# Kernel tuning notes

Measured on AMD Instinct MI355X. Metric: run time of the kernel, lower is better.

The kernel has to match this reference:

```python
import jax, jax.numpy as jnp
from jax import lax
import numpy as np


def _conv2d(x, w, b, pad):
    # x: NCHW, w: OIHW
    o = lax.conv_general_dilated(x, w, window_strides=(1, 1),
                                 padding=[(pad, pad), (pad, pad)],
                                 dimension_numbers=('NCHW', 'OIHW', 'NCHW'))
    return o + b[None, :, None, None]


def _maxpool(x, kh, kw):
    return lax.reduce_window(x, -jnp.inf, lax.max,
                             window_dimensions=(1, 1, kh, kw),
                             window_strides=(1, 1, kh, kw),
                             padding='VALID')


def _l2norm(x, axis):
    n = jnp.sqrt(jnp.sum(x * x, axis=axis, keepdims=True))
    return x / jnp.maximum(n, 1e-12)


def setup_inputs() -> dict:
    key = jax.random.key(0)
    ks = jax.random.split(key, 12)
    d = {}
    d['x'] = jax.random.normal(ks[0], (16, 128, 40, 200), dtype=jnp.float32)
    d['cluster_centers'] = jax.random.uniform(ks[1], (64, 128), dtype=jnp.float32)
    d['conv_w'] = jax.random.normal(ks[2], (64, 128, 1, 1), dtype=jnp.float32) * 0.05
    d['conv_b'] = jax.random.normal(ks[3], (64,), dtype=jnp.float32) * 0.05
    d['w1'] = jax.random.normal(ks[4], (256, 128, 5, 5), dtype=jnp.float32) * 0.02
    d['b1'] = jax.random.normal(ks[5], (256,), dtype=jnp.float32) * 0.02
    d['w2'] = jax.random.normal(ks[6], (512, 256, 5, 5), dtype=jnp.float32) * 0.02
    d['b2'] = jax.random.normal(ks[7], (512,), dtype=jnp.float32) * 0.02
    d['w3'] = jax.random.normal(ks[8], (1024, 512, 5, 5), dtype=jnp.float32) * 0.02
    d['b3'] = jax.random.normal(ks[9], (1024,), dtype=jnp.float32) * 0.02
    d['mlp_w'] = jax.random.normal(ks[10], (256, 9216), dtype=jnp.float32) * 0.01
    d['mlp_b'] = jax.random.normal(ks[11], (256,), dtype=jnp.float32) * 0.01
    return d


def reference(x, cluster_centers, conv_w, conv_b, w1, b1, w2, b2, w3, b3, mlp_w, mlp_b):
    N, C, H, W = x.shape
    K = conv_w.shape[0]
    P = H * W

    # soft assignment: 1x1 conv -> softmax over cluster axis
    sa = _conv2d(x, conv_w, conv_b, 0).reshape(N, K, P)
    a = jax.nn.softmax(sa, axis=1)                      # [N, K, P]

    x_flat = x.reshape(N, C, P)
    # sum_p a[n,k,p] * (x[n,c,p] - centers[k,c])  -- algebraically equal to
    # the explicit NxKxCxP residual tensor, computed without materializing it.
    vlad = jnp.einsum('nkp,ncp->nkc', a, x_flat) \
           - a.sum(axis=-1)[:, :, None] * cluster_centers[None, :, :]
    vlad = _l2norm(vlad, axis=2)                        # intra-norm per cluster
    vlad = _l2norm(vlad.reshape(N, K * C), axis=1)      # [N, K*C]

    # CNN branch
    h = _conv2d(x, w1, b1, 2)
    h = jnp.where(h >= 0, h, 0.2 * h)                   # LeakyReLU(0.2)
    h = _maxpool(h, 2, 2)
    h = _conv2d(h, w2, b2, 2)
    h = jnp.where(h >= 0, h, 0.2 * h)
    h = _maxpool(h, 4, 4)
    h = _conv2d(h, w3, b3, 2)
    h = _maxpool(h, 5, 25)                              # -> [N, 1024, 1, 1]
    x_feat = _l2norm(h.reshape(N, -1), axis=1)          # [N, 1024]

    feat = jnp.concatenate([vlad, x_feat], axis=1)      # [N, 9216]
    out = feat @ mlp_w.T + mlp_b
    return _l2norm(out, axis=1)
```

## Files before the change

### kernel.cpp

```cpp
#include <hip/hip_runtime.h>
#include <math.h>

#define K_ 64
#define C_ 128
#define NB 16
#define P_ 8000

typedef float f32x4 __attribute__((ext_vector_type(4)));
typedef short s16x8 __attribute__((ext_vector_type(8)));

__device__ __forceinline__ short f2bf(float v) {
    unsigned u = __float_as_uint(v);
    u += 0x7FFFu + ((u >> 16) & 1u);
    return (short)(u >> 16);
}
__device__ __forceinline__ float bf2f(ushort u) { return __uint_as_float(((unsigned)u) << 16); }

__device__ __forceinline__ void stage16(const void* g, void* l) {
    __builtin_amdgcn_global_load_lds(
        (const __attribute__((address_space(1))) void*)g,
        (__attribute__((address_space(3))) void*)l, 16, 0, 0);
}

__global__ void k_transpose_tiled(const float* __restrict__ in, float* __restrict__ out,
                                  int Co, int E)
{
    __shared__ float t[32][33];
    const int e0  = blockIdx.x * 32;
    const int co0 = blockIdx.y * 32;
    for (int i = threadIdx.y; i < 32; i += 8) {
        int co = co0 + i, e = e0 + threadIdx.x;
        t[i][threadIdx.x] = (co < Co && e < E) ? in[(size_t)co * E + e] : 0.f;
    }
    __syncthreads();
    for (int i = threadIdx.y; i < 32; i += 8) {
        int e = e0 + i, co = co0 + threadIdx.x;
        if (e < E && co < Co) out[(size_t)e * Co + co] = t[threadIdx.x][i];
    }
}

__global__ void k_nchw_to_nhwc(const float* __restrict__ in, ushort* __restrict__ out,
                               int C, int P)
{
    __shared__ ushort t[32][33];
    const int n  = blockIdx.z;
    const int p0 = blockIdx.x * 32;
    const int c0 = blockIdx.y * 32;
    for (int i = threadIdx.y; i < 32; i += 8) {
        int c = c0 + i, p = p0 + threadIdx.x;
        t[i][threadIdx.x] = (c < C && p < P) ? (ushort)f2bf(in[((size_t)n * C + c) * P + p]) : 0;
    }
    __syncthreads();
    for (int i = threadIdx.y; i < 32; i += 8) {
        int p = p0 + i, c = c0 + threadIdx.x;
        if (p < P && c < C) out[((size_t)n * P + p) * C + c] = t[threadIdx.x][i];
    }
}

__global__ void k_wprep(const float* __restrict__ w, short* __restrict__ wb,
                        int Co, int Cin, int total)
{
    int idx = blockIdx.x * blockDim.x + threadIdx.x;
    if (idx >= total) return;
    int cl = idx & 31;
    int rest = idx >> 5;
    int co = rest % Co;
    int rest2 = rest / Co;
    int t = rest2 % 25;
    int ck = rest2 / 25;
    float v = w[((size_t)co * Cin + (ck << 5) + cl) * 25 + t];
    wb[idx] = f2bf(v);
}

template<int SR, int NC, int WR, int WC16, int IS3>
__global__ __launch_bounds__(256) void k_conv_mfma(
    const ushort* __restrict__ in, const s16x8* __restrict__ wb,
    const float* __restrict__ bias, ushort* __restrict__ outb, float* __restrict__ outf,
    const ushort* __restrict__ zg,
    int Cin, int Co, int H, int W, int WT, int leaky, int nck, int xpc, int PT)
{
    constexpr int NT   = IS3 ? 4 : (WR * WC16);
    constexpr int TOT  = SR * NC * 4;
    constexpr int TOTP = (TOT + 63) & ~63;
    __shared__ s16x8 xin[TOTP];
    __shared__ s16x8 wl[2][4][256];

    const int tid  = threadIdx.x;
    const int lane = tid & 63;
    const int wid  = tid >> 6;
    const int wm   = wid >> 1;
    const int wn   = wid & 1;
    const int n16  = lane & 15;
    const int g    = lane >> 4;

    const int lid  = blockIdx.x;
    const int xcd  = lid & 7;
    const int rrr  = lid >> 3;
    const int co_blk = xcd / xpc;
    const int posn = rrr * xpc + (xcd % xpc);
    const int n    = posn / PT;
    const int bx   = posn % PT;

    const int h0  = IS3 ? 0 : (bx / WT) * (2 * WR);
    const int w0  = IS3 ? 0 : (bx % WT) * (WC16 * 16);
    const int ks  = IS3 ? bx : 0;
    const int co0 = co_blk * 128;

    int ph[NT], pw[NT];
    if (IS3) {
        #pragma unroll
        for (int nt = 0; nt < NT; ++nt) {
            int pos = wn * 64 + nt * 16 + n16;
            int h = pos / 25;
            int w = pos - h * 25;
            if (h > 4) { h = 0; w = 0; }
            ph[nt] = h; pw[nt] = w;
        }
    }

    f32x4 acc[4][NT];
    #pragma unroll
    for (int i = 0; i < 4; ++i)
        #pragma unroll
        for (int j = 0; j < NT; ++j) acc[i][j] = f32x4{0.f, 0.f, 0.f, 0.f};

    const int ck0 = IS3 ? ks * nck : 0;
    const int ckend = ck0 + nck;

    auto stage_input = [&](int ck) {
        for (int c = wid; c * 64 < TOTP; c += 4) {
            int u = c * 64 + lane;
            int row = u / (NC * 4);
            int rem = u - row * (NC * 4);
            int col = rem >> 2;
            int s   = rem & 3;
            int g8  = (s - (col >> 1) - row) & 3;
            int gh = h0 + row - 2, gw = w0 + col - 2;
            const void* src =
                (u < TOT && (unsigned)gh < (unsigned)H && (unsigned)gw < (unsigned)W)
                ? (const void*)(in + ((size_t)(n * H + gh) * W + gw) * Cin + (ck << 5) + (g8 << 3))
                : (const void*)zg;
            stage16(src, (void*)&xin[c * 64]);
        }
    };
    auto stage_w = [&](int gT, int slot) {
        const s16x8* src = wb + ((size_t)gT * Co + co0 + wm * 64) * 4 + lane;
        #pragma unroll
        for (int k = 0; k < 4; ++k)
            stage16((const void*)(src + k * 64), (void*)&wl[slot][wid][k * 64]);
    };

    for (int ck = ck0; ck < ckend; ++ck) {
        if (ck != ck0) __builtin_amdgcn_s_barrier();
        stage_input(ck);
        stage_w(ck * 25, 0);
        asm volatile("s_waitcnt vmcnt(4)" ::: "memory");
        __builtin_amdgcn_sched_barrier(0);
        __builtin_amdgcn_s_barrier();

        #pragma unroll
        for (int t = 0; t < 25; ++t) {
            if (t < 24) {
                stage_w(ck * 25 + t + 1, (t + 1) & 1);
                asm volatile("s_waitcnt vmcnt(4)" ::: "memory");
            } else {
                asm volatile("s_waitcnt vmcnt(0)" ::: "memory");
            }
            __builtin_amdgcn_sched_barrier(0);

            const int r = t / 5, s = t - (t / 5) * 5;

            const s16x8* wt_ = &wl[t & 1][wid][n16 * 4 + g];
            s16x8 wf[4];
            #pragma unroll
            for (int mt = 0; mt < 4; ++mt) wf[mt] = wt_[mt * 64];

            s16x8 bf[NT];
            #pragma unroll
            for (int nt = 0; nt < NT; ++nt) {
                int row, col;
                if (IS3) { row = ph[nt] + r; col = pw[nt] + s; }
                else {
                    int rr = nt / WC16, cc = nt - rr * WC16;
                    row = wn * WR + rr + r;
                    col = cc * 16 + n16 + s;
                }
                bf[nt] = xin[(row * NC + col) * 4 + ((g + (col >> 1) + row) & 3)];
            }
            #pragma unroll
            for (int mt = 0; mt < 4; ++mt)
                #pragma unroll
                for (int nt = 0; nt < NT; ++nt)
                    acc[mt][nt] = __builtin_amdgcn_mfma_f32_16x16x32_bf16(
                        wf[mt], bf[nt], acc[mt][nt], 0, 0, 0);
        }
    }

    if (IS3) {
        #pragma unroll
        for (int mt = 0; mt < 4; ++mt) {
            #pragma unroll
            for (int reg = 0; reg < 4; ++reg) {
                const int co = co0 + wm * 64 + mt * 16 + g * 4 + reg;
                #pragma unroll
                for (int nt = 0; nt < NT; ++nt) {
                    int pos = wn * 64 + nt * 16 + n16;
                    if (pos < 125)
                        outf[((size_t)(ks * NB + n) * Co + co) * 125 + pos] = acc[mt][nt][reg];
                }
            }
        }
    } else {
        #pragma unroll
        for (int mt = 0; mt < 4; ++mt) {
            const int cobase = co0 + wm * 64 + mt * 16 + g * 4;
            const float b0 = bias[cobase + 0];
            const float b1 = bias[cobase + 1];
            const float b2 = bias[cobase + 2];
            const float b3 = bias[cobase + 3];
            #pragma unroll
            for (int nt = 0; nt < NT; ++nt) {
                int rr = nt / WC16, cc = nt - rr * WC16;
                int h  = h0 + wn * WR + rr;
                int wp = w0 + cc * 16 + n16;
                if (h < H && wp < W) {
                    float v0 = acc[mt][nt][0] + b0;
                    float v1 = acc[mt][nt][1] + b1;
                    float v2 = acc[mt][nt][2] + b2;
                    float v3 = acc[mt][nt][3] + b3;
                    if (leaky) {
                        v0 = (v0 >= 0.f) ? v0 : 0.2f * v0;
                        v1 = (v1 >= 0.f) ? v1 : 0.2f * v1;
                        v2 = (v2 >= 0.f) ? v2 : 0.2f * v2;
                        v3 = (v3 >= 0.f) ? v3 : 0.2f * v3;
                    }
                    ushort4 pkd;
                    pkd.x = (ushort)f2bf(v0);
                    pkd.y = (ushort)f2bf(v1);
                    pkd.z = (ushort)f2bf(v2);
                    pkd.w = (ushort)f2bf(v3);
                    *(ushort4*)(outb + ((size_t)(n * H + h) * W + wp) * Co + cobase) = pkd;
                }
            }
        }
    }
}

__global__ __launch_bounds__(256) void k_vlad_partial(
    const float* __restrict__ x,
    const float* __restrict__ convw_t,
    const float* __restrict__ convb,
    float* __restrict__ pv,
    float* __restrict__ pa)
{
    __shared__ float xs[C_][64];
    __shared__ float als[64][K_];
    __shared__ float pgsum[4][K_];

    const int tid = threadIdx.x;
    const int chunk = blockIdx.x;
    const int n = blockIdx.y;
    const int p0 = chunk * 64;

    const float* xn = x + (size_t)n * C_ * P_ + p0;
    for (int i = tid; i < C_ * 64; i += 256) {
        int c = i >> 6, pp = i & 63;
        xs[c][pp] = xn[(size_t)c * P_ + pp];
    }
    __syncthreads();

    const int k  = tid & 63;
    const int pg = tid >> 6;

    float sa[16];
    const float bk = convb[k];
    #pragma unroll
    for (int j = 0; j < 16; ++j) sa[j] = bk;
    for (int c = 0; c < C_; ++c) {
        float wv = convw_t[c * K_ + k];
        const float4* xp = (const float4*)&xs[c][pg * 16];
        #pragma unroll
        for (int q = 0; q < 4; ++q) {
            float4 xv = xp[q];
            sa[q*4+0] += wv * xv.x;
            sa[q*4+1] += wv * xv.y;
            sa[q*4+2] += wv * xv.z;
            sa[q*4+3] += wv * xv.w;
        }
    }

    float asum_loc = 0.f;
    #pragma unroll
    for (int j = 0; j < 16; ++j) {
        float m = sa[j];
        for (int d = 32; d >= 1; d >>= 1) m = fmaxf(m, __shfl_xor(m, d));
        float e = __expf(sa[j] - m);
        float s = e;
        for (int d = 32; d >= 1; d >>= 1) s += __shfl_xor(s, d);
        float a = e / s;
        als[pg * 16 + j][k] = a;
        asum_loc += a;
    }
    pgsum[pg][k] = asum_loc;
    __syncthreads();
    if (tid < K_) {
        pa[((size_t)n * 125 + chunk) * K_ + tid] =
            pgsum[0][tid] + pgsum[1][tid] + pgsum[2][tid] + pgsum[3][tid];
    }

    const int q = pg;
    float acc[32];
    #pragma unroll
    for (int j = 0; j < 32; ++j) acc[j] = 0.f;
    for (int p = 0; p < 64; p += 4) {
        float a0 = als[p+0][k], a1 = als[p+1][k], a2 = als[p+2][k], a3 = als[p+3][k];
        #pragma unroll
        for (int j = 0; j < 32; ++j) {
            const float4 xv = *(const float4*)&xs[q*32 + j][p];
            acc[j] += a0*xv.x + a1*xv.y + a2*xv.z + a3*xv.w;
        }
    }
    float* pvp = pv + ((((size_t)n * 125 + chunk) * K_ + k) * C_ + q * 32);
    #pragma unroll
    for (int j = 0; j < 32; ++j) pvp[j] = acc[j];
}

__global__ void k_vlad_reduce(const float* __restrict__ pv, float* __restrict__ vlad_raw)
{
    int idx = blockIdx.x * blockDim.x + threadIdx.x;
    if (idx >= NB * 8192) return;
    int n = idx >> 13;
    int rest = idx & 8191;
    const float* p = pv + (size_t)n * 125 * 8192 + rest;
    float s = 0.f;
    for (int ch = 0; ch < 125; ++ch) s += p[(size_t)ch * 8192];
    vlad_raw[(size_t)n * 8192 + rest] = s;
}

__global__ void k_asum_reduce(const float* __restrict__ pa, float* __restrict__ asum)
{
    int idx = blockIdx.x * blockDim.x + threadIdx.x;
    if (idx >= NB * K_) return;
    const float* p = pa + (size_t)(idx >> 6) * 125 * K_ + (idx & 63);
    float s = 0.f;
    for (int ch = 0; ch < 125; ++ch) s += p[ch * K_];
    asum[idx] = s;
}

__global__ __launch_bounds__(128) void k_vlad_finalize(
    const float* __restrict__ vlad_raw, const float* __restrict__ asum,
    const float* __restrict__ centers, float* __restrict__ feat)
{
    __shared__ float red[2];
    const int k = blockIdx.x, n = blockIdx.y, c = threadIdx.x;
    float v = vlad_raw[((size_t)n * K_ + k) * C_ + c] - asum[n * K_ + k] * centers[k * C_ + c];
    float ss = v * v;
    for (int d = 32; d >= 1; d >>= 1) ss += __shfl_xor(ss, d);
    if ((threadIdx.x & 63) == 0) red[threadIdx.x >> 6] = ss;
    __syncthreads();
    float denom = fmaxf(sqrtf(red[0] + red[1]), 1e-12f);
    feat[(size_t)n * 9216 + k * C_ + c] = v / denom;
}

__global__ void k_maxpool_cl(const ushort* __restrict__ in, ushort* __restrict__ out,
                             int Hi, int Wi, int C8, int ph, int pw, int total)
{
    int idx = blockIdx.x * blockDim.x + threadIdx.x;
    if (idx >= total) return;
    const int Ho = Hi / ph, Wo = Wi / pw;
    const int C = C8 << 3;
    int c8 = idx % C8;
    int t  = idx / C8;
    int wo = t % Wo; t /= Wo;
    int ho = t % Ho;
    int n  = t / Ho;
    const ushort* base = in + ((size_t)(n * Hi + ho * ph) * Wi + wo * pw) * C + (c8 << 3);
    float m[8];
    #pragma unroll
    for (int j = 0; j < 8; ++j) m[j] = -INFINITY;
    for (int r = 0; r < ph; ++r)
        for (int s = 0; s < pw; ++s) {
            s16x8 v = *(const s16x8*)(base + ((size_t)r * Wi + s) * C);
            #pragma unroll
            for (int j = 0; j < 8; ++j) m[j] = fmaxf(m[j], bf2f((ushort)v[j]));
        }
    s16x8 o;
    #pragma unroll
    for (int j = 0; j < 8; ++j) o[j] = f2bf(m[j]);
    *(s16x8*)(out + ((size_t)(n * Ho + ho) * Wo + wo) * C + (c8 << 3)) = o;
}

__global__ void k_pool3_feat(const float* __restrict__ part, const float* __restrict__ bias,
                             float* __restrict__ feat)
{
    int idx = blockIdx.x * blockDim.x + threadIdx.x;
    if (idx >= NB * 1024) return;
    int n = idx >> 10, c = idx & 1023;
    const size_t kstride = (size_t)NB * 1024 * 125;
    const float* p0 = part + ((size_t)n * 1024 + c) * 125;
    const float* p1 = p0 + kstride;
    const float* p2 = p1 + kstride;
    const float* p3 = p2 + kstride;
    const float b = bias[c];
    float m = -INFINITY;
    for (int i = 0; i < 125; ++i)
        m = fmaxf(m, b + ((p0[i] + p1[i]) + (p2[i] + p3[i])));
    feat[(size_t)n * 9216 + 8192 + c] = m;
}

__global__ __launch_bounds__(256) void k_featnorm(const float* __restrict__ feat,
                                                  float* __restrict__ scale)
{
    __shared__ float r1s[4], r2s[4];
    const int n = blockIdx.x;
    const int tid = threadIdx.x;
    const int wid = tid >> 6;
    float s1 = 0.f, s2 = 0.f;
    const float* f = feat + (size_t)n * 9216;
    for (int i = tid; i < 9216; i += 256) {
        float v = f[i];
        if (i < 8192) s1 += v * v; else s2 += v * v;
    }
    for (int d = 32; d >= 1; d >>= 1) { s1 += __shfl_xor(s1, d); s2 += __shfl_xor(s2, d); }
    if ((tid & 63) == 0) { r1s[wid] = s1; r2s[wid] = s2; }
    __syncthreads();
    if (tid == 0) {
        scale[n * 2 + 0] = 1.f / fmaxf(sqrtf(r1s[0] + r1s[1] + r1s[2] + r1s[3]), 1e-12f);
        scale[n * 2 + 1] = 1.f / fmaxf(sqrtf(r2s[0] + r2s[1] + r2s[2] + r2s[3]), 1e-12f);
    }
}

__global__ __launch_bounds__(256) void k_mlp_part(
    const float* __restrict__ feat, const float* __restrict__ scale,
    const float* __restrict__ wt,
    float* __restrict__ part)
{
    __shared__ float fs[576];
    const int n  = blockIdx.x >> 4;
    const int sl = blockIdx.x & 15;
    const int tid = threadIdx.x;
    const int base = sl * 576;
    for (int j = tid; j < 576; j += 256) {
        int idx = base + j;
        fs[j] = feat[(size_t)n * 9216 + idx] * scale[n * 2 + (idx < 8192 ? 0 : 1)];
    }
    __syncthreads();
    float a0 = 0.f, a1 = 0.f;
    for (int j = 0; j < 576; j += 2) {
        a0 += fs[j]     * wt[(size_t)(base + j)     * 256 + tid];
        a1 += fs[j + 1] * wt[(size_t)(base + j + 1) * 256 + tid];
    }
    part[((size_t)n * 16 + sl) * 256 + tid] = a0 + a1;
}

__global__ __launch_bounds__(256) void k_mlp_final(
    const float* __restrict__ part, const float* __restrict__ bias,
    float* __restrict__ outp)
{
    __shared__ float red[4];
    const int n = blockIdx.x;
    const int tid = threadIdx.x;
    float a = bias[tid];
    #pragma unroll
    for (int s = 0; s < 16; ++s) a += part[((size_t)n * 16 + s) * 256 + tid];
    float ss = a * a;
    for (int d = 32; d >= 1; d >>= 1) ss += __shfl_xor(ss, d);
    if ((tid & 63) == 0) red[tid >> 6] = ss;
    __syncthreads();
    const float inv = 1.f / fmaxf(sqrtf(red[0] + red[1] + red[2] + red[3]), 1e-12f);
    outp[n * 256 + tid] = a * inv;
}

extern "C" void kernel_launch(void* const* d_in, const int* in_sizes, int n_in,
                              void* d_out, int out_size, void* d_ws, size_t ws_size,
                              hipStream_t stream)
{
    const float* x      = (const float*)d_in[0];
    const float* cents  = (const float*)d_in[1];
    const float* conv_w = (const float*)d_in[2];
    const float* conv_b = (const float*)d_in[3];
    const float* w1     = (const float*)d_in[4];
    const float* b1     = (const float*)d_in[5];
    const float* w2     = (const float*)d_in[6];
    const float* b2     = (const float*)d_in[7];
    const float* w3     = (const float*)d_in[8];
    const float* b3     = (const float*)d_in[9];
    const float* mlp_w  = (const float*)d_in[10];
    const float* mlp_b  = (const float*)d_in[11];
    float* outp = (float*)d_out;

    char* ws = (char*)d_ws;
    size_t off = 0;
    auto alloc = [&](size_t bytes) -> void* {
        off = (off + 255) & ~(size_t)255;
        void* p = ws + off;
        off += bytes;
        return p;
    };
    ushort* zguard  = (ushort*)alloc(256);
    float*  convw_t = (float*)alloc((size_t)64 * 128 * 4);
    float*  mwt     = (float*)alloc((size_t)9216 * 256 * 4);
    short*  wb1     = (short*)alloc((size_t)819200 * 2);
    short*  wb2     = (short*)alloc((size_t)3276800 * 2);
    short*  wb3     = (short*)alloc((size_t)13107200 * 2);
    ushort* x_cl    = (ushort*)alloc((size_t)NB * 8000 * 128 * 2);
    float*  vlad_raw= (float*)alloc((size_t)NB * 8192 * 4);
    float*  asum    = (float*)alloc((size_t)NB * K_ * 4);
    float*  feat    = (float*)alloc((size_t)NB * 9216 * 4);
    float*  pa      = (float*)alloc((size_t)NB * 125 * K_ * 4);
    float*  scale   = (float*)alloc((size_t)NB * 2 * 4);
    float*  mpart   = (float*)alloc((size_t)NB * 16 * 256 * 4);
    ushort* pool2b  = (ushort*)alloc((size_t)NB * 125 * 512 * 2);
    float*  part3   = (float*)alloc((size_t)4 * NB * 1024 * 125 * 4);
    char*   slabA   = (char*)alloc((size_t)NB * 8000 * 256 * 2);
    ushort* slabB   = (ushort*)alloc((size_t)NB * 2000 * 256 * 2);

    hipMemsetAsync(zguard, 0, 256, stream);

    {
        dim3 blk(32, 8);
        k_transpose_tiled<<<dim3(4, 2), blk, 0, stream>>>(conv_w, convw_t, 64, 128);
        k_transpose_tiled<<<dim3(288, 8), blk, 0, stream>>>(mlp_w, mwt, 256, 9216);
        k_wprep<<<(819200 + 255) / 256, 256, 0, stream>>>(w1, wb1, 256, 128, 819200);
        k_wprep<<<(3276800 + 255) / 256, 256, 0, stream>>>(w2, wb2, 512, 256, 3276800);
        k_wprep<<<(13107200 + 255) / 256, 256, 0, stream>>>(w3, wb3, 1024, 512, 13107200);
        k_nchw_to_nhwc<<<dim3(250, 4, NB), blk, 0, stream>>>(x, x_cl, 128, 8000);
    }

    k_vlad_partial<<<dim3(125, NB), 256, 0, stream>>>(x, convw_t, conv_b, (float*)slabA, pa);
    k_vlad_reduce<<<(NB * 8192 + 255) / 256, 256, 0, stream>>>((float*)slabA, vlad_raw);
    k_asum_reduce<<<(NB * K_ + 255) / 256, 256, 0, stream>>>(pa, asum);
    k_vlad_finalize<<<dim3(K_, NB), 128, 0, stream>>>(vlad_raw, asum, cents, feat);

    k_conv_mfma<12, 36, 4, 2, 0><<<1120, 256, 0, stream>>>(
        x_cl, (const s16x8*)wb1, b1, (ushort*)slabA, nullptr, zguard,
        128, 256, 40, 200, 7, 1, 4, 4, 35);
    {
        int tot = NB * 20 * 100 * 32;
        k_maxpool_cl<<<(tot + 255) / 256, 256, 0, stream>>>(
            (ushort*)slabA, slabB, 40, 200, 32, 2, 2, tot);
    }
    k_conv_mfma<8, 68, 2, 4, 0><<<640, 256, 0, stream>>>(
        slabB, (const s16x8*)wb2, b2, (ushort*)slabA, nullptr, zguard,
        256, 512, 20, 100, 2, 1, 8, 2, 10);
    {
        int tot = NB * 5 * 25 * 64;
        k_maxpool_cl<<<(tot + 255) / 256, 256, 0, stream>>>(
            (ushort*)slabA, pool2b, 20, 100, 64, 4, 4, tot);
    }
    k_conv_mfma<9, 29, 4, 1, 1><<<512, 256, 0, stream>>>(
        pool2b, (const s16x8*)wb3, b3, nullptr, part3, zguard,
        512, 1024, 5, 25, 1, 0, 4, 1, 4);
    k_pool3_feat<<<(NB * 1024 + 255) / 256, 256, 0, stream>>>(part3, b3, feat);

    k_featnorm<<<NB, 256, 0, stream>>>(feat, scale);
    k_mlp_part<<<NB * 16, 256, 0, stream>>>(feat, scale, mwt, mpart);
    k_mlp_final<<<NB, 256, 0, stream>>>(mpart, mlp_b, outp);
}
```

Measured before the change: 1.133 ms.

## Retile MFMA conv blocks to 256 output channels with waves split over channels

The conv kernel's four waves now each own 64 output channels and the whole spatial tile, instead of a 2x2 split over channels and rows. Each block therefore covers 256 output channels over a smaller spatial tile. All three conv launches get new template and grid parameters. Conv3's K-split goes from 4 to 8 slices, with partial sums reduced in pool3_feat, and the partial buffer reuses slabA. MFMA bursts are wrapped in s_setprio. The aim is more input-tile reuse per staged block and fewer redundant input loads, at the cost of more accumulator registers (NT up to 8) and more K-split partial traffic.

```diff
diff --git a/kernel.cpp b/kernel.cpp
--- a/kernel.cpp
+++ b/kernel.cpp
@@ -79,7 +79,7 @@
     const ushort* __restrict__ zg,
     int Cin, int Co, int H, int W, int WT, int leaky, int nck, int xpc, int PT)
 {
-    constexpr int NT   = IS3 ? 4 : (WR * WC16);
+    constexpr int NT   = IS3 ? 8 : (WR * WC16);
     constexpr int TOT  = SR * NC * 4;
     constexpr int TOTP = (TOT + 63) & ~63;
     __shared__ s16x8 xin[TOTP];
@@ -88,8 +88,7 @@
     const int tid  = threadIdx.x;
     const int lane = tid & 63;
     const int wid  = tid >> 6;
-    const int wm   = wid >> 1;
-    const int wn   = wid & 1;
+    const int wm   = wid;
     const int n16  = lane & 15;
     const int g    = lane >> 4;
 
@@ -101,16 +100,16 @@
     const int n    = posn / PT;
     const int bx   = posn % PT;
 
-    const int h0  = IS3 ? 0 : (bx / WT) * (2 * WR);
+    const int h0  = IS3 ? 0 : (bx / WT) * WR;
     const int w0  = IS3 ? 0 : (bx % WT) * (WC16 * 16);
     const int ks  = IS3 ? bx : 0;
-    const int co0 = co_blk * 128;
+    const int co0 = co_blk * 256;
 
     int ph[NT], pw[NT];
     if (IS3) {
         #pragma unroll
         for (int nt = 0; nt < NT; ++nt) {
-            int pos = wn * 64 + nt * 16 + n16;
+            int pos = nt * 16 + n16;
             int h = pos / 25;
             int w = pos - h * 25;
             if (h > 4) { h = 0; w = 0; }
@@ -182,17 +181,19 @@
                 if (IS3) { row = ph[nt] + r; col = pw[nt] + s; }
                 else {
                     int rr = nt / WC16, cc = nt - rr * WC16;
-                    row = wn * WR + rr + r;
+                    row = rr + r;
                     col = cc * 16 + n16 + s;
                 }
                 bf[nt] = xin[(row * NC + col) * 4 + ((g + (col >> 1) + row) & 3)];
             }
+            __builtin_amdgcn_s_setprio(1);
             #pragma unroll
             for (int mt = 0; mt < 4; ++mt)
                 #pragma unroll
                 for (int nt = 0; nt < NT; ++nt)
                     acc[mt][nt] = __builtin_amdgcn_mfma_f32_16x16x32_bf16(
                         wf[mt], bf[nt], acc[mt][nt], 0, 0, 0);
+            __builtin_amdgcn_s_setprio(0);
         }
     }
 
@@ -204,7 +205,7 @@
                 const int co = co0 + wm * 64 + mt * 16 + g * 4 + reg;
                 #pragma unroll
                 for (int nt = 0; nt < NT; ++nt) {
-                    int pos = wn * 64 + nt * 16 + n16;
+                    int pos = nt * 16 + n16;
                     if (pos < 125)
                         outf[((size_t)(ks * NB + n) * Co + co) * 125 + pos] = acc[mt][nt][reg];
                 }
@@ -221,7 +222,7 @@
             #pragma unroll
             for (int nt = 0; nt < NT; ++nt) {
                 int rr = nt / WC16, cc = nt - rr * WC16;
-                int h  = h0 + wn * WR + rr;
+                int h  = h0 + rr;
                 int wp = w0 + cc * 16 + n16;
                 if (h < H && wp < W) {
                     float v0 = acc[mt][nt][0] + b0;
@@ -397,14 +398,15 @@
     if (idx >= NB * 1024) return;
     int n = idx >> 10, c = idx & 1023;
     const size_t kstride = (size_t)NB * 1024 * 125;
-    const float* p0 = part + ((size_t)n * 1024 + c) * 125;
-    const float* p1 = p0 + kstride;
-    const float* p2 = p1 + kstride;
-    const float* p3 = p2 + kstride;
+    const float* p = part + ((size_t)n * 1024 + c) * 125;
     const float b = bias[c];
     float m = -INFINITY;
-    for (int i = 0; i < 125; ++i)
-        m = fmaxf(m, b + ((p0[i] + p1[i]) + (p2[i] + p3[i])));
+    for (int i = 0; i < 125; ++i) {
+        float s = 0.f;
+        #pragma unroll
+        for (int ksl = 0; ksl < 8; ++ksl) s += p[i + ksl * kstride];
+        m = fmaxf(m, b + s);
+    }
     feat[(size_t)n * 9216 + 8192 + c] = m;
 }
 
@@ -511,8 +513,7 @@
     float*  scale   = (float*)alloc((size_t)NB * 2 * 4);
     float*  mpart   = (float*)alloc((size_t)NB * 16 * 256 * 4);
     ushort* pool2b  = (ushort*)alloc((size_t)NB * 125 * 512 * 2);
-    float*  part3   = (float*)alloc((size_t)4 * NB * 1024 * 125 * 4);
-    char*   slabA   = (char*)alloc((size_t)NB * 8000 * 256 * 2);
+    char*   slabA   = (char*)alloc((size_t)8 * NB * 1024 * 125 * 4);
     ushort* slabB   = (ushort*)alloc((size_t)NB * 2000 * 256 * 2);
 
     hipMemsetAsync(zguard, 0, 256, stream);
@@ -532,26 +533,26 @@
     k_asum_reduce<<<(NB * K_ + 255) / 256, 256, 0, stream>>>(pa, asum);
     k_vlad_finalize<<<dim3(K_, NB), 128, 0, stream>>>(vlad_raw, asum, cents, feat);
 
-    k_conv_mfma<12, 36, 4, 2, 0><<<1120, 256, 0, stream>>>(
+    k_conv_mfma<8, 36, 4, 2, 0><<<1120, 256, 0, stream>>>(
         x_cl, (const s16x8*)wb1, b1, (ushort*)slabA, nullptr, zguard,
-        128, 256, 40, 200, 7, 1, 4, 4, 35);
+        128, 256, 40, 200, 7, 1, 4, 8, 70);
     {
         int tot = NB * 20 * 100 * 32;
         k_maxpool_cl<<<(tot + 255) / 256, 256, 0, stream>>>(
             (ushort*)slabA, slabB, 40, 200, 32, 2, 2, tot);
     }
-    k_conv_mfma<8, 68, 2, 4, 0><<<640, 256, 0, stream>>>(
+    k_conv_mfma<8, 36, 4, 2, 0><<<640, 256, 0, stream>>>(
         slabB, (const s16x8*)wb2, b2, (ushort*)slabA, nullptr, zguard,
-        256, 512, 20, 100, 2, 1, 8, 2, 10);
+        256, 512, 20, 100, 4, 1, 8, 4, 20);
     {
         int tot = NB * 5 * 25 * 64;
         k_maxpool_cl<<<(tot + 255) / 256, 256, 0, stream>>>(
             (ushort*)slabA, pool2b, 20, 100, 64, 4, 4, tot);
     }
-    k_conv_mfma<9, 29, 4, 1, 1><<<512, 256, 0, stream>>>(
-        pool2b, (const s16x8*)wb3, b3, nullptr, part3, zguard,
-        512, 1024, 5, 25, 1, 0, 4, 1, 4);
-    k_pool3_feat<<<(NB * 1024 + 255) / 256, 256, 0, stream>>>(part3, b3, feat);
+    k_conv_mfma<9, 29, 4, 2, 1><<<512, 256, 0, stream>>>(
+        pool2b, (const s16x8*)wb3, b3, nullptr, (float*)slabA, zguard,
+        512, 1024, 5, 25, 1, 0, 2, 2, 8);
+    k_pool3_feat<<<(NB * 1024 + 255) / 256, 256, 0, stream>>>((float*)slabA, b3, feat);
 
     k_featnorm<<<NB, 256, 0, stream>>>(feat, scale);
     k_mlp_part<<<NB * 16, 256, 0, stream>>>(feat, scale, mwt, mpart);
```

After: 1.141 ms. About the same (+0.7%).
